# Performance work log

Measured on AMD Instinct MI355X. Metric: run time of the kernel, lower is better.

The kernel has to match this reference:

```python
import jax, jax.numpy as jnp
import numpy as np

B, S, D, H = 4, 1024, 1024, 16
DK = D // H


def setup_inputs() -> dict:
    key = jax.random.key(0)
    ks = jax.random.split(key, 14)
    scale = 1.0 / np.sqrt(D)
    inp = {
        "Qx": jax.random.normal(ks[0], (B, S, D), jnp.float32),
        "Kx": jax.random.normal(ks[1], (B, S, D), jnp.float32),
        "Vx": jax.random.normal(ks[2], (B, S, D), jnp.float32),
        "prob_phn": jax.random.uniform(ks[3], (B, S, S), jnp.float32),
        "mask": jax.random.randint(ks[4], (B, S, S), 0, 2, jnp.int32),
        "lambda_val": 1,
        "Wq": jax.random.normal(ks[5], (D, D), jnp.float32) * scale,
        "bq": jnp.zeros((D,), jnp.float32),
        "Wk": jax.random.normal(ks[6], (D, D), jnp.float32) * scale,
        "bk": jnp.zeros((D,), jnp.float32),
        "Wv": jax.random.normal(ks[7], (D, D), jnp.float32) * scale,
        "bv": jnp.zeros((D,), jnp.float32),
        "Wo": jax.random.normal(ks[8], (D, D), jnp.float32) * scale,
        "bo": jnp.zeros((D,), jnp.float32),
    }
    return inp


def _split_heads(x):
    # [B,S,D] -> [B,H,S,DK]
    b, s, _ = x.shape
    return x.reshape(b, s, H, DK).transpose(0, 2, 1, 3)


def reference(Qx, Kx, Vx, prob_phn, mask, lambda_val, Wq, bq, Wk, bk, Wv, bv, Wo, bo):
    q = _split_heads(Qx @ Wq.T + bq)
    k = _split_heads(Kx @ Wk.T + bk)
    v = _split_heads(Vx @ Wv.T + bv)
    scores = jnp.einsum("bhqd,bhkd->bhqk", q, k) / jnp.sqrt(jnp.float32(DK))
    if lambda_val > 0:
        # prob_phn: [B,S,S] -> transpose last two dims, broadcast over heads
        scores = scores - lambda_val * jnp.swapaxes(prob_phn, -2, -1)[:, None]
    scores = jnp.where(mask[:, None] == 0, jnp.float32(-1e9), scores)
    probs = jax.nn.softmax(scores, axis=-1)
    attn = jnp.einsum("bhqk,bhkd->bhqd", probs, v)
    out = attn.transpose(0, 2, 1, 3).reshape(Qx.shape[0], Qx.shape[1], D)
    out = out @ Wo.T + bo
    return (out, mask)
```

## Files before the change

### kernel.cpp

```cpp
#include <hip/hip_runtime.h>
#include <hip/hip_bf16.h>
#include <cstdint>
#include <cstddef>

#define BB 4
#define SS 1024
#define DD 1024
#define HH 16
#define DKK 64

typedef unsigned short u16;
typedef __bf16 bf16_t;
typedef __attribute__((ext_vector_type(8))) bf16_t bf16x8;
typedef __attribute__((ext_vector_type(4))) float floatx4;

#define LOG2E 1.4426950408889634f
#define QKSCALE 0.18033688011112042f

static __device__ inline u16 f2bf(float f) {
    union { float f; unsigned u; } v; v.f = f;
    unsigned r = v.u + 0x7fffu + ((v.u >> 16) & 1u);
    return (u16)(r >> 16);
}

static __device__ inline void load16_lds(const void* g, void* l) {
    __builtin_amdgcn_global_load_lds(
        (const __attribute__((address_space(1))) unsigned int*)g,
        (__attribute__((address_space(3))) unsigned int*)l,
        16, 0, 0);
}

static __device__ inline int swz64(int row, int c) { return row * 64 + ((c ^ (row & 7)) * 8); }
static __device__ inline int swz32(int row, int c) { return row * 32 + ((c ^ ((row >> 1) & 3)) * 8); }

static __device__ inline float lam_val(const int* p) {
    int v = *p;
    if (v >= -100000 && v <= 100000) return (float)v;
    union { int i; float f; } u; u.i = v; return u.f;
}

__global__ void prep_kernel(const float* __restrict__ Qx, const float* __restrict__ Kx,
                            const float* __restrict__ Vx,
                            const float* __restrict__ Wq, const float* __restrict__ Wk,
                            const float* __restrict__ Wv, const float* __restrict__ Wo,
                            const float* __restrict__ prob, const int* __restrict__ mask,
                            const int* __restrict__ lam_p,
                            u16* __restrict__ Xq, u16* __restrict__ Xk, u16* __restrict__ Xv,
                            u16* __restrict__ wq, u16* __restrict__ wk,
                            u16* __restrict__ wv, u16* __restrict__ wo,
                            u16* __restrict__ biasT, float* __restrict__ maskOut)
{
    __shared__ float tile[64][65];
    __shared__ u16 btile[64][68];
    const int blk = blockIdx.x, tid = threadIdx.x;

    if (blk >= 1024) {
        const int cb = blk - 1024;
        const int base = cb * 1024;
        const float* src; u16* dst; int off0;
        if (base < 3145728) {
            int s = base >> 20;  off0 = base & 1048575;
            src = (s == 0) ? Qx : (s == 1) ? Kx : Vx;
            dst = (s == 0) ? Xq : (s == 1) ? Xk : Xv;
        } else {
            int v2 = base - 3145728;
            int s = v2 >> 18;  off0 = v2 & 262143;
            src = (s == 0) ? Wq : (s == 1) ? Wk : (s == 2) ? Wv : Wo;
            dst = (s == 0) ? wq : (s == 1) ? wk : (s == 2) ? wv : wo;
        }
        float4 f[4];
        #pragma unroll
        for (int r = 0; r < 4; ++r)
            f[r] = ((const float4*)src)[off0 + r * 256 + tid];
        #pragma unroll
        for (int r = 0; r < 4; ++r) {
            ushort4 o;
            o.x = f2bf(f[r].x); o.y = f2bf(f[r].y);
            o.z = f2bf(f[r].z); o.w = f2bf(f[r].w);
            ((ushort4*)dst)[off0 + r * 256 + tid] = o;
        }
        return;
    }

    const int b = blk >> 8;
    const int q0 = ((blk >> 4) & 15) * 64, k0 = (blk & 15) * 64;
    const int kt = blk & 15;
    #pragma unroll
    for (int rr = 0; rr < 4; ++rr) {
        int unit = rr * 256 + tid;
        int kl = unit >> 4, qi = unit & 15;
        float4 p4 = *(const float4*)&prob[((size_t)(b * SS + k0 + kl)) * SS + q0 + qi * 4];
        tile[kl][qi * 4 + 0] = p4.x;
        tile[kl][qi * 4 + 1] = p4.y;
        tile[kl][qi * 4 + 2] = p4.z;
        tile[kl][qi * 4 + 3] = p4.w;
    }
    __syncthreads();
    const float lamc = lam_val(lam_p) * LOG2E;
    #pragma unroll
    for (int rr = 0; rr < 4; ++rr) {
        int pair = rr * 256 + tid;
        int q = pair >> 4, k4 = pair & 15;
        size_t midx = ((size_t)(b * SS + q0 + q)) * SS + k0 + k4 * 4;
        int4 m4 = *(const int4*)&mask[midx];
        float p0 = tile[k4 * 4 + 0][q];
        float p1 = tile[k4 * 4 + 1][q];
        float p2 = tile[k4 * 4 + 2][q];
        float p3 = tile[k4 * 4 + 3][q];
        ushort4 bb;
        bb.x = f2bf((m4.x == 0) ? -1.5e9f : -lamc * p0);
        bb.y = f2bf((m4.y == 0) ? -1.5e9f : -lamc * p1);
        bb.z = f2bf((m4.z == 0) ? -1.5e9f : -lamc * p2);
        bb.w = f2bf((m4.w == 0) ? -1.5e9f : -lamc * p3);
        *(ushort4*)&btile[q][k4 * 4] = bb;
        if (maskOut) {
            float4 mf = { (float)m4.x, (float)m4.y, (float)m4.z, (float)m4.w };
            *(float4*)&maskOut[midx] = mf;
        }
    }
    __syncthreads();
    u16* bT = biasT + (size_t)(b * 16 + kt) * 65536;
    #pragma unroll
    for (int rr = 0; rr < 4; ++rr) {
        int idx = rr * 256 + tid;
        int j = idx >> 8, quad = (idx >> 6) & 3, ql = idx & 63;
        ushort4 v = *(const ushort4*)&btile[ql][j * 16 + quad * 4];
        *(ushort4*)&bT[(size_t)((j * 4 + quad) * 1024 + q0 + ql) * 4] = v;
    }
}

template <int MODE>
static __device__ inline void gemm_body(const u16* __restrict__ A, const u16* __restrict__ W,
                                        const float* __restrict__ bias,
                                        u16* __restrict__ Cb, float* __restrict__ Cf)
{
    constexpr int K = 1024, N = 1024;
    __shared__ __align__(16) u16 As[128 * 32];
    __shared__ __align__(16) u16 Bs[128 * 32];
    const int tid = threadIdx.x;
    const int wv = tid >> 6, ln = tid & 63, l15 = ln & 15, quad = ln >> 4;
    const int mBase = blockIdx.y * 128;
    const int nBase = blockIdx.x * 128;
    const int wm = (wv & 1) * 64, wn = (wv >> 1) * 64;

    const u16* Aptr[2]; const u16* Wptr[2];
    #pragma unroll
    for (int r = 0; r < 2; ++r) {
        int p = r * 256 + wv * 64 + ln;
        int row = p >> 2;
        int c = (p & 3) ^ ((row >> 1) & 3);
        Aptr[r] = A + (size_t)(mBase + row) * K + c * 8;
        Wptr[r] = W + (size_t)(nBase + row) * K + c * 8;
    }

    floatx4 acc[4][4] = {};

    for (int k0 = 0; k0 < K; k0 += 32) {
        __syncthreads();
        #pragma unroll
        for (int r = 0; r < 2; ++r) {
            load16_lds(Aptr[r] + k0, &As[(r * 256 + wv * 64) * 8]);
            load16_lds(Wptr[r] + k0, &Bs[(r * 256 + wv * 64) * 8]);
        }
        __syncthreads();
        bf16x8 af[4], bfr[4];
        #pragma unroll
        for (int i = 0; i < 4; ++i)
            af[i] = *(const bf16x8*)&As[swz32(wm + i * 16 + l15, quad)];
        #pragma unroll
        for (int j = 0; j < 4; ++j)
            bfr[j] = *(const bf16x8*)&Bs[swz32(wn + j * 16 + l15, quad)];
        #pragma unroll
        for (int i = 0; i < 4; ++i)
            #pragma unroll
            for (int j = 0; j < 4; ++j)
                acc[i][j] = __builtin_amdgcn_mfma_f32_16x16x32_bf16(af[i], bfr[j], acc[i][j], 0, 0, 0);
    }

    #pragma unroll
    for (int i = 0; i < 4; ++i) {
        #pragma unroll
        for (int j = 0; j < 4; ++j) {
            int col = nBase + wn + j * 16 + l15;
            float bcol = bias[col];
            if (MODE == 2) {
                int hh = col >> 6, dk = col & 63;
                int row0 = mBase + wm + i * 16 + quad * 4;
                int bb = row0 >> 10, s = row0 & 1023;
                ushort4 v4;
                v4.x = f2bf(acc[i][j][0] + bcol);
                v4.y = f2bf(acc[i][j][1] + bcol);
                v4.z = f2bf(acc[i][j][2] + bcol);
                v4.w = f2bf(acc[i][j][3] + bcol);
                *(ushort4*)&Cb[((size_t)((bb * HH + hh) * DKK) + dk) * SS + s] = v4;
            } else {
                #pragma unroll
                for (int r = 0; r < 4; ++r) {
                    int row = mBase + wm + i * 16 + quad * 4 + r;
                    float v = acc[i][j][r] + bcol;
                    if (MODE == 1) Cf[(size_t)row * N + col] = v;
                    else           Cb[(size_t)row * N + col] = f2bf(v);
                }
            }
        }
    }
}

__global__ __launch_bounds__(256) void gemm_qkv_kernel(
    const u16* __restrict__ Xq, const u16* __restrict__ Xk, const u16* __restrict__ Xv,
    const u16* __restrict__ Wq, const u16* __restrict__ Wk, const u16* __restrict__ Wv,
    const float* __restrict__ bq, const float* __restrict__ bk, const float* __restrict__ bv,
    u16* __restrict__ Cq, u16* __restrict__ Ck, u16* __restrict__ Vtout)
{
    const int z = blockIdx.z;
    if (z == 2) {
        gemm_body<2>(Xv, Wv, bv, Vtout, nullptr);
    } else {
        const u16* A = (z == 0) ? Xq : Xk;
        const u16* W = (z == 0) ? Wq : Wk;
        const float* bias = (z == 0) ? bq : bk;
        u16* C = (z == 0) ? Cq : Ck;
        gemm_body<0>(A, W, bias, C, nullptr);
    }
}

__global__ __launch_bounds__(256) void gemm_out_kernel(
    const u16* __restrict__ A, const u16* __restrict__ W,
    const float* __restrict__ bias, float* __restrict__ Cf)
{
    gemm_body<1>(A, W, bias, nullptr, Cf);
}

__global__ __launch_bounds__(256) void attn_kernel(
    const u16* __restrict__ Qf, const u16* __restrict__ Kf,
    const u16* __restrict__ Vt, const u16* __restrict__ biasT,
    u16* __restrict__ Attn)
{
    __shared__ __align__(16) u16 Qs[64 * 64];
    __shared__ __align__(16) u16 Ks[64 * 64];
    __shared__ __align__(16) u16 Vs[64 * 64];
    __shared__ __align__(16) u16 Ps[4][16 * 72];
    const int tid = threadIdx.x;
    const int wv = tid >> 6, ln = tid & 63, l15 = ln & 15, quad = ln >> 4;

    const int lin = blockIdx.x + 16 * blockIdx.y + 256 * blockIdx.z;
    const int sw  = (lin & 7) * 128 + (lin >> 3);
    const int qt = sw & 15, h = (sw >> 4) & 15, b = sw >> 8;
    const int q0 = qt * 64;

    int row64[2], col64[2];
    #pragma unroll
    for (int r = 0; r < 2; ++r) {
        int p = r * 256 + wv * 64 + ln;
        row64[r] = p >> 3;
        col64[r] = ((p & 7) ^ (row64[r] & 7)) * 8;
    }

    #pragma unroll
    for (int r = 0; r < 2; ++r)
        load16_lds(Qf + ((size_t)(b * SS + q0 + row64[r])) * DD + h * DKK + col64[r],
                   &Qs[(r * 256 + wv * 64) * 8]);
    __syncthreads();

    bf16x8 aq[2];
    #pragma unroll
    for (int t = 0; t < 2; ++t)
        aq[t] = *(const bf16x8*)&Qs[swz64(wv * 16 + l15, t * 4 + quad)];

    const size_t vt_head = ((size_t)(b * HH + h)) * DKK * SS;
    const u16* Kp[2]; const u16* Vp[2];
    #pragma unroll
    for (int r = 0; r < 2; ++r) {
        Kp[r] = Kf + ((size_t)(b * SS + row64[r])) * DD + h * DKK + col64[r];
        Vp[r] = Vt + vt_head + (size_t)row64[r] * SS + col64[r];
    }

    const int qq = q0 + wv * 16 + l15;
    const u16* bpT = biasT + (size_t)b * 1048576 + (size_t)quad * 4096 + (size_t)qq * 4;

    floatx4 o[4] = {};
    float rsum = 0.f;

    for (int kt = 0; kt < 16; ++kt) {
        const int kk0 = kt * 64;
        __syncthreads();
        #pragma unroll
        for (int r = 0; r < 2; ++r) {
            load16_lds(Kp[r] + (size_t)kk0 * DD, &Ks[(r * 256 + wv * 64) * 8]);
            load16_lds(Vp[r] + kk0, &Vs[(r * 256 + wv * 64) * 8]);
        }
        __syncthreads();

        uint2 braw[4];
        #pragma unroll
        for (int j = 0; j < 4; ++j)
            braw[j] = *(const uint2*)&bpT[(size_t)kt * 65536 + j * 16384];

        floatx4 sfr[4];
        #pragma unroll
        for (int j = 0; j < 4; ++j) {
            bf16x8 bk0 = *(const bf16x8*)&Ks[swz64(j * 16 + l15, quad)];
            bf16x8 bk1 = *(const bf16x8*)&Ks[swz64(j * 16 + l15, 4 + quad)];
            floatx4 s = {};
            s = __builtin_amdgcn_mfma_f32_16x16x32_bf16(bk0, aq[0], s, 0, 0, 0);
            sfr[j] = __builtin_amdgcn_mfma_f32_16x16x32_bf16(bk1, aq[1], s, 0, 0, 0);
        }

        #pragma unroll
        for (int j = 0; j < 4; ++j) {
            float b0 = __uint_as_float(braw[j].x << 16);
            float b1 = __uint_as_float(braw[j].x & 0xffff0000u);
            float b2 = __uint_as_float(braw[j].y << 16);
            float b3 = __uint_as_float(braw[j].y & 0xffff0000u);
            float p0 = __builtin_amdgcn_exp2f(fmaf(sfr[j][0], QKSCALE, b0));
            float p1 = __builtin_amdgcn_exp2f(fmaf(sfr[j][1], QKSCALE, b1));
            float p2 = __builtin_amdgcn_exp2f(fmaf(sfr[j][2], QKSCALE, b2));
            float p3 = __builtin_amdgcn_exp2f(fmaf(sfr[j][3], QKSCALE, b3));
            rsum += (p0 + p1) + (p2 + p3);
            uint2 pk;
            pk.x = (__float_as_uint(p0) >> 16) | (__float_as_uint(p1) & 0xffff0000u);
            pk.y = (__float_as_uint(p2) >> 16) | (__float_as_uint(p3) & 0xffff0000u);
            *(uint2*)&Ps[wv][l15 * 72 + j * 16 + quad * 4] = pk;
        }

        #pragma unroll
        for (int t = 0; t < 2; ++t) {
            bf16x8 ap = *(const bf16x8*)&Ps[wv][l15 * 72 + t * 32 + quad * 8];
            #pragma unroll
            for (int j = 0; j < 4; ++j) {
                bf16x8 bvv = *(const bf16x8*)&Vs[swz64(j * 16 + l15, t * 4 + quad)];
                o[j] = __builtin_amdgcn_mfma_f32_16x16x32_bf16(bvv, ap, o[j], 0, 0, 0);
            }
        }
    }

    rsum += __shfl_xor(rsum, 16);
    rsum += __shfl_xor(rsum, 32);
    const float ri = 1.0f / rsum;

    u16* outp = Attn + ((size_t)(b * SS + qq)) * DD + h * DKK + quad * 4;
    #pragma unroll
    for (int j = 0; j < 4; ++j) {
        ushort4 v4;
        v4.x = f2bf(o[j][0] * ri);
        v4.y = f2bf(o[j][1] * ri);
        v4.z = f2bf(o[j][2] * ri);
        v4.w = f2bf(o[j][3] * ri);
        *(ushort4*)&outp[j * 16] = v4;
    }
}

extern "C" void kernel_launch(void* const* d_in, const int* in_sizes, int n_in,
                              void* d_out, int out_size, void* d_ws, size_t ws_size,
                              hipStream_t stream)
{
    const float* Qx  = (const float*)d_in[0];
    const float* Kx  = (const float*)d_in[1];
    const float* Vx  = (const float*)d_in[2];
    const float* prob = (const float*)d_in[3];
    const int*   mask = (const int*)d_in[4];
    const int*   lam  = (const int*)d_in[5];
    const float* Wq  = (const float*)d_in[6];
    const float* bq  = (const float*)d_in[7];
    const float* Wk  = (const float*)d_in[8];
    const float* bk  = (const float*)d_in[9];
    const float* Wv  = (const float*)d_in[10];
    const float* bv  = (const float*)d_in[11];
    const float* Wo  = (const float*)d_in[12];
    const float* bo  = (const float*)d_in[13];

    char* ws = (char*)d_ws;
    const size_t MB = 1024 * 1024;
    u16*   Xq     = (u16*)(ws + 0 * MB);
    u16*   Xk     = (u16*)(ws + 8 * MB);
    u16*   Xv     = (u16*)(ws + 16 * MB);
    u16*   wq     = (u16*)(ws + 24 * MB);
    u16*   wk     = (u16*)(ws + 26 * MB);
    u16*   wvp    = (u16*)(ws + 28 * MB);
    u16*   wo     = (u16*)(ws + 30 * MB);
    u16*   q_flat = (u16*)(ws + 32 * MB);
    u16*   k_flat = (u16*)(ws + 40 * MB);
    u16*   vt     = (u16*)(ws + 56 * MB);
    u16*   biasT  = (u16*)(ws + 64 * MB);
    u16*   attn   = (u16*)(ws + 80 * MB);

    float* maskOut = (out_size >= 2 * BB * SS * DD) ? (float*)d_out + (size_t)BB * SS * DD
                                                    : nullptr;

    prep_kernel<<<5120, 256, 0, stream>>>(Qx, Kx, Vx, Wq, Wk, Wv, Wo, prob, mask, lam,
                                          Xq, Xk, Xv, wq, wk, wvp, wo, biasT, maskOut);
    gemm_qkv_kernel<<<dim3(8, 32, 3), 256, 0, stream>>>(Xq, Xk, Xv, wq, wk, wvp,
                                                        bq, bk, bv, q_flat, k_flat, vt);
    attn_kernel<<<dim3(16, 16, 4), 256, 0, stream>>>(q_flat, k_flat, vt, biasT, attn);
    gemm_out_kernel<<<dim3(8, 32, 1), 256, 0, stream>>>(attn, wo, bo, (float*)d_out);
}
```

Baseline: 258.8 us.

## Double GEMM K-tile to 64, swizzle block order for XCDs, widen prep stores

The GEMM main loop now stages 64-wide K slices instead of 32 in LDS, using a 64-column XOR swizzle. This halves the number of barrier pairs per output tile. The QKV and output-projection kernels remap linear block IDs so that blocks placed on the same XCD work on neighbouring tiles, which should improve L2 reuse. The fp32-to-bf16 conversion path also writes 16-byte stores instead of 8-byte ones. The cost is double the LDS per block, which may lower occupancy.

```diff
diff --git a/kernel.cpp b/kernel.cpp
--- a/kernel.cpp
+++ b/kernel.cpp
@@ -31,7 +31,6 @@
 }
 
 static __device__ inline int swz64(int row, int c) { return row * 64 + ((c ^ (row & 7)) * 8); }
-static __device__ inline int swz32(int row, int c) { return row * 32 + ((c ^ ((row >> 1) & 3)) * 8); }
 
 static __device__ inline float lam_val(const int* p) {
     int v = *p;
@@ -68,16 +67,18 @@
             src = (s == 0) ? Wq : (s == 1) ? Wk : (s == 2) ? Wv : Wo;
             dst = (s == 0) ? wq : (s == 1) ? wk : (s == 2) ? wv : wo;
         }
-        float4 f[4];
-        #pragma unroll
-        for (int r = 0; r < 4; ++r)
-            f[r] = ((const float4*)src)[off0 + r * 256 + tid];
-        #pragma unroll
-        for (int r = 0; r < 4; ++r) {
-            ushort4 o;
-            o.x = f2bf(f[r].x); o.y = f2bf(f[r].y);
-            o.z = f2bf(f[r].z); o.w = f2bf(f[r].w);
-            ((ushort4*)dst)[off0 + r * 256 + tid] = o;
+        const float4* s4 = (const float4*)src;
+        #pragma unroll
+        for (int r = 0; r < 2; ++r) {
+            int i4 = off0 + r * 512 + tid * 2;
+            float4 a  = s4[i4];
+            float4 b2 = s4[i4 + 1];
+            uint4 pk;
+            pk.x = (unsigned)f2bf(a.x)  | ((unsigned)f2bf(a.y)  << 16);
+            pk.y = (unsigned)f2bf(a.z)  | ((unsigned)f2bf(a.w)  << 16);
+            pk.z = (unsigned)f2bf(b2.x) | ((unsigned)f2bf(b2.y) << 16);
+            pk.w = (unsigned)f2bf(b2.z) | ((unsigned)f2bf(b2.w) << 16);
+            *(uint4*)((ushort4*)dst + i4) = pk;
         }
         return;
     }
@@ -132,49 +133,51 @@
 template <int MODE>
 static __device__ inline void gemm_body(const u16* __restrict__ A, const u16* __restrict__ W,
                                         const float* __restrict__ bias,
-                                        u16* __restrict__ Cb, float* __restrict__ Cf)
+                                        u16* __restrict__ Cb, float* __restrict__ Cf,
+                                        int mBase, int nBase)
 {
     constexpr int K = 1024, N = 1024;
-    __shared__ __align__(16) u16 As[128 * 32];
-    __shared__ __align__(16) u16 Bs[128 * 32];
+    __shared__ __align__(16) u16 As[128 * 64];
+    __shared__ __align__(16) u16 Bs[128 * 64];
     const int tid = threadIdx.x;
     const int wv = tid >> 6, ln = tid & 63, l15 = ln & 15, quad = ln >> 4;
-    const int mBase = blockIdx.y * 128;
-    const int nBase = blockIdx.x * 128;
     const int wm = (wv & 1) * 64, wn = (wv >> 1) * 64;
 
-    const u16* Aptr[2]; const u16* Wptr[2];
-    #pragma unroll
-    for (int r = 0; r < 2; ++r) {
+    const u16* Aptr[4]; const u16* Wptr[4];
+    #pragma unroll
+    for (int r = 0; r < 4; ++r) {
         int p = r * 256 + wv * 64 + ln;
-        int row = p >> 2;
-        int c = (p & 3) ^ ((row >> 1) & 3);
+        int row = p >> 3;
+        int c = (p & 7) ^ (row & 7);
         Aptr[r] = A + (size_t)(mBase + row) * K + c * 8;
         Wptr[r] = W + (size_t)(nBase + row) * K + c * 8;
     }
 
     floatx4 acc[4][4] = {};
 
-    for (int k0 = 0; k0 < K; k0 += 32) {
+    for (int k0 = 0; k0 < K; k0 += 64) {
         __syncthreads();
         #pragma unroll
-        for (int r = 0; r < 2; ++r) {
+        for (int r = 0; r < 4; ++r) {
             load16_lds(Aptr[r] + k0, &As[(r * 256 + wv * 64) * 8]);
             load16_lds(Wptr[r] + k0, &Bs[(r * 256 + wv * 64) * 8]);
         }
         __syncthreads();
-        bf16x8 af[4], bfr[4];
-        #pragma unroll
-        for (int i = 0; i < 4; ++i)
-            af[i] = *(const bf16x8*)&As[swz32(wm + i * 16 + l15, quad)];
-        #pragma unroll
-        for (int j = 0; j < 4; ++j)
-            bfr[j] = *(const bf16x8*)&Bs[swz32(wn + j * 16 + l15, quad)];
-        #pragma unroll
-        for (int i = 0; i < 4; ++i)
+        #pragma unroll
+        for (int t = 0; t < 2; ++t) {
+            bf16x8 af[4], bfr[4];
+            #pragma unroll
+            for (int i = 0; i < 4; ++i)
+                af[i] = *(const bf16x8*)&As[swz64(wm + i * 16 + l15, t * 4 + quad)];
             #pragma unroll
             for (int j = 0; j < 4; ++j)
-                acc[i][j] = __builtin_amdgcn_mfma_f32_16x16x32_bf16(af[i], bfr[j], acc[i][j], 0, 0, 0);
+                bfr[j] = *(const bf16x8*)&Bs[swz64(wn + j * 16 + l15, t * 4 + quad)];
+            #pragma unroll
+            for (int i = 0; i < 4; ++i)
+                #pragma unroll
+                for (int j = 0; j < 4; ++j)
+                    acc[i][j] = __builtin_amdgcn_mfma_f32_16x16x32_bf16(af[i], bfr[j], acc[i][j], 0, 0, 0);
+        }
     }
 
     #pragma unroll
@@ -212,15 +215,19 @@
     const float* __restrict__ bq, const float* __restrict__ bk, const float* __restrict__ bv,
     u16* __restrict__ Cq, u16* __restrict__ Ck, u16* __restrict__ Vtout)
 {
-    const int z = blockIdx.z;
+    const int lin = blockIdx.x + 8 * blockIdx.y + 256 * blockIdx.z;
+    const int sw  = (lin & 7) * 96 + (lin >> 3);
+    const int x = sw & 7, y = (sw >> 3) & 31, z = sw >> 8;
+    const int mBase = y * 128, nBase = x * 128;
+
     if (z == 2) {
-        gemm_body<2>(Xv, Wv, bv, Vtout, nullptr);
+        gemm_body<2>(Xv, Wv, bv, Vtout, nullptr, mBase, nBase);
     } else {
         const u16* A = (z == 0) ? Xq : Xk;
         const u16* W = (z == 0) ? Wq : Wk;
         const float* bias = (z == 0) ? bq : bk;
         u16* C = (z == 0) ? Cq : Ck;
-        gemm_body<0>(A, W, bias, C, nullptr);
+        gemm_body<0>(A, W, bias, C, nullptr, mBase, nBase);
     }
 }
 
@@ -228,7 +235,10 @@
     const u16* __restrict__ A, const u16* __restrict__ W,
     const float* __restrict__ bias, float* __restrict__ Cf)
 {
-    gemm_body<1>(A, W, bias, nullptr, Cf);
+    const int lin = blockIdx.x + 8 * blockIdx.y;
+    const int sw  = (lin & 7) * 32 + (lin >> 3);
+    const int x = sw & 7, y = sw >> 3;
+    gemm_body<1>(A, W, bias, nullptr, Cf, y * 128, x * 128);
 }
 
 __global__ __launch_bounds__(256) void attn_kernel(
```

After: 252.7 us. 2.3% less time.
